# Kernel tuning notes

Hardware: AMD Instinct MI355X
Metric: run time of the kernel (lower is better)

## Reference

```python
import jax, jax.numpy as jnp
import numpy as np

NUM_NODES = 100000
NUM_EDGES = 50000
NUM_CONN = 800000
IN_DIM = 256
HIDDEN = 128
EDGE_ATTR_DIM = 17
LN_EPS = 1e-5


def setup_inputs() -> dict:
    key = jax.random.key(0)
    k1, k2, k3, kw1, kb1, kg, kbeta, kw2, kb2 = jax.random.split(key, 9)
    node_features = jax.random.normal(k1, (NUM_NODES, IN_DIM), dtype=jnp.float32)
    nodes = jax.random.randint(k2, (NUM_CONN,), 0, NUM_NODES, dtype=jnp.int64)
    edges = jax.random.randint(k3, (NUM_CONN,), 0, NUM_EDGES, dtype=jnp.int64)
    hyperedge_index = jnp.stack([nodes, edges], axis=0)
    # MLP params (Linear(in,hid) -> LayerNorm -> ReLU -> Dropout(eval:identity) -> Linear(hid,out))
    W1 = jax.random.normal(kw1, (IN_DIM, HIDDEN), dtype=jnp.float32) * (1.0 / np.sqrt(IN_DIM))
    b1 = jax.random.normal(kb1, (HIDDEN,), dtype=jnp.float32) * 0.01
    ln_g = jnp.ones((HIDDEN,), dtype=jnp.float32)
    ln_b = jnp.zeros((HIDDEN,), dtype=jnp.float32)
    W2 = jax.random.normal(kw2, (HIDDEN, EDGE_ATTR_DIM), dtype=jnp.float32) * (1.0 / np.sqrt(HIDDEN))
    b2 = jax.random.normal(kb2, (EDGE_ATTR_DIM,), dtype=jnp.float32) * 0.01
    return {"node_features": node_features, "hyperedge_index": hyperedge_index,
            "W1": W1, "b1": b1, "ln_g": ln_g, "ln_b": ln_b, "W2": W2, "b2": b2}


def reference(node_features, hyperedge_index, W1, b1, ln_g, ln_b, W2, b2):
    nodes = hyperedge_index[0]
    edges = hyperedge_index[1]
    # indices are in-range by construction (torch valid_mask is all-True here)
    gathered = node_features[nodes]                         # [num_conn, in_dim]
    summed = jax.ops.segment_sum(gathered, edges, num_segments=NUM_EDGES)
    counts = jax.ops.segment_sum(jnp.ones(edges.shape, node_features.dtype), edges,
                                 num_segments=NUM_EDGES)
    edge_features = summed / jnp.clip(counts, 1.0)[:, None]  # mean aggregation
    # decoder MLP (dropout inactive in eval)
    h = edge_features @ W1 + b1
    mu = jnp.mean(h, axis=-1, keepdims=True)
    var = jnp.mean(jnp.square(h - mu), axis=-1, keepdims=True)
    h = (h - mu) * jax.lax.rsqrt(var + LN_EPS) * ln_g + ln_b
    h = jax.nn.relu(h)
    return h @ W2 + b2                                      # [num_edges, edge_attr_dim]
```

## Files before the change

### kernel.cpp

```cpp
#include <hip/hip_runtime.h>
#include <hip/hip_bf16.h>
#include <stdint.h>

#define NUM_NODES 100000
#define NUM_EDGES 50000
#define NUM_CONN  800000
#define IN_DIM    256
#define HIDDEN    128
#define EDGE_DIM  17
#define PAD       64
#define CSTRIDE   16

typedef __bf16 bf16x8 __attribute__((ext_vector_type(8)));
typedef float  f32x4  __attribute__((ext_vector_type(4)));


__global__ void prep_kernel(const float* __restrict__ W1, const float* __restrict__ W2,
                            __bf16* __restrict__ w1f, __bf16* __restrict__ w2f,
                            int* __restrict__ counts2) {
    int i = blockIdx.x * 256 + threadIdx.x;
    if (i < NUM_EDGES) {
        int4 z = {0, 0, 0, 0};
        int4* c4 = (int4*)(counts2 + (size_t)i * CSTRIDE);
        c4[0] = z; c4[1] = z; c4[2] = z; c4[3] = z;
    }
    if (i < 4096) {
        int lane = i & 63, t = (i >> 6) & 7, kc2 = i >> 9;
        int m = lane & 15, q = lane >> 4;
        int n = t * 16 + m;
        int kbase = kc2 * 32 + q * 8;
        __bf16* dst = w1f + (size_t)i * 8;
        #pragma unroll
        for (int ki = 0; ki < 8; ++ki)
            dst[ki] = (__bf16)W1[(size_t)(kbase + ki) * HIDDEN + n];
    } else if (i < 4608) {
        int f = i - 4096;
        int lane = f & 63, t = (f >> 6) & 1, ks = f >> 7;
        int m = lane & 15, q = lane >> 4;
        int n = t * 16 + m;
        int kbase = ks * 32 + q * 8;
        __bf16* dst = w2f + (size_t)f * 8;
        #pragma unroll
        for (int ki = 0; ki < 8; ++ki)
            dst[ki] = (n < EDGE_DIM) ? (__bf16)W2[(size_t)(kbase + ki) * EDGE_DIM + n]
                                     : (__bf16)0.0f;
    }
}

#define FRONT_BLOCKS 2346
__global__ __launch_bounds__(256, 4) void front_kernel(const int* __restrict__ idx,
        int stride, int* __restrict__ counts2, int* __restrict__ slots,
        const float* __restrict__ nf, const __bf16* __restrict__ w1f,
        __bf16* __restrict__ pbf) {
    __shared__ __align__(16) __bf16 lds_w[16384];
    const int nb = blockIdx.x / 3, r3 = blockIdx.x % 3;
    if (r3 == 1) {
        long c0 = ((long)nb * 256 + threadIdx.x) * 4;
        if (c0 < NUM_CONN) {
            int nd[4], ed[4];
            if (stride == 2) {
                #pragma unroll
                for (int k = 0; k < 2; ++k) {
                    int4 vn = ((const int4*)idx)[c0 / 2 + k];
                    int4 ve = ((const int4*)(idx + 2 * NUM_CONN))[c0 / 2 + k];
                    nd[2 * k] = vn.x; nd[2 * k + 1] = vn.z;
                    ed[2 * k] = ve.x; ed[2 * k + 1] = ve.z;
                }
            } else {
                #pragma unroll
                for (int k = 0; k < 4; ++k) {
                    nd[k] = idx[c0 + k];
                    ed[k] = idx[NUM_CONN + c0 + k];
                }
            }
            int pos[4];
            #pragma unroll
            for (int k = 0; k < 4; ++k)
                pos[k] = atomicAdd(&counts2[(size_t)ed[k] * CSTRIDE], 1);
            #pragma unroll
            for (int k = 0; k < 4; ++k)
                if (pos[k] < PAD) slots[(size_t)ed[k] * PAD + pos[k]] = nd[k];
        }
        return;
    }
    const int p = 2 * nb + (r3 == 2 ? 1 : 0);
    const int wave = threadIdx.x >> 6;
    const int lane = threadIdx.x & 63;
    const int m = lane & 15, q = lane >> 4;
    int row = p * 64 + wave * 16 + m;
    if (row >= NUM_NODES) row = NUM_NODES - 1;
    const float* ap = nf + (size_t)row * IN_DIM + q * 8;

    const uint4* src = (const uint4*)w1f;
    uint4* dst = (uint4*)lds_w;

    bf16x8 afr[8];
    {
        float4 a4[8];
        #pragma unroll
        for (int kc2 = 0; kc2 < 4; ++kc2) {
            a4[2 * kc2]     = *(const float4*)(ap + kc2 * 32);
            a4[2 * kc2 + 1] = *(const float4*)(ap + kc2 * 32 + 4);
        }
        #pragma unroll
        for (int i = threadIdx.x; i < 2048; i += 256) {
            int kc2 = i >> 8, tt = (i >> 6) & 3, l = i & 63;
            dst[i] = src[(kc2 * 8 + tt) * 64 + l];
        }
        #pragma unroll
        for (int kc2 = 0; kc2 < 4; ++kc2) {
            float4 f0 = a4[2 * kc2], f1 = a4[2 * kc2 + 1];
            afr[kc2][0] = (__bf16)f0.x; afr[kc2][1] = (__bf16)f0.y;
            afr[kc2][2] = (__bf16)f0.z; afr[kc2][3] = (__bf16)f0.w;
            afr[kc2][4] = (__bf16)f1.x; afr[kc2][5] = (__bf16)f1.y;
            afr[kc2][6] = (__bf16)f1.z; afr[kc2][7] = (__bf16)f1.w;
        }
        #pragma unroll
        for (int kc2 = 4; kc2 < 8; ++kc2) {
            a4[2 * (kc2 - 4)]     = *(const float4*)(ap + kc2 * 32);
            a4[2 * (kc2 - 4) + 1] = *(const float4*)(ap + kc2 * 32 + 4);
        }
        #pragma unroll
        for (int kc2 = 4; kc2 < 8; ++kc2) {
            float4 f0 = a4[2 * (kc2 - 4)], f1 = a4[2 * (kc2 - 4) + 1];
            afr[kc2][0] = (__bf16)f0.x; afr[kc2][1] = (__bf16)f0.y;
            afr[kc2][2] = (__bf16)f0.z; afr[kc2][3] = (__bf16)f0.w;
            afr[kc2][4] = (__bf16)f1.x; afr[kc2][5] = (__bf16)f1.y;
            afr[kc2][6] = (__bf16)f1.z; afr[kc2][7] = (__bf16)f1.w;
        }
    }
    __syncthreads();

    const bf16x8* frag = (const bf16x8*)lds_w;
    #pragma unroll
    for (int ph = 0; ph < 2; ++ph) {
        f32x4 acc[4];
        #pragma unroll
        for (int tt = 0; tt < 4; ++tt) acc[tt] = (f32x4){0.f, 0.f, 0.f, 0.f};
        #pragma unroll
        for (int kc2 = 0; kc2 < 8; ++kc2) {
            #pragma unroll
            for (int tt = 0; tt < 4; ++tt)
                acc[tt] = __builtin_amdgcn_mfma_f32_16x16x32_bf16(
                    afr[kc2], frag[(kc2 * 4 + tt) * 64 + lane], acc[tt], 0, 0, 0);
        }
        int ob = p * 64 + wave * 16 + q * 4;
        #pragma unroll
        for (int tt = 0; tt < 4; ++tt) {
            int col = (ph * 4 + tt) * 16 + m;
            #pragma unroll
            for (int r = 0; r < 4; ++r) {
                int orow = ob + r;
                if (orow < NUM_NODES)
                    pbf[(size_t)orow * HIDDEN + col] = (__bf16)acc[tt][r];
            }
        }
        if (ph == 0) {
            __syncthreads();
            #pragma unroll
            for (int i = threadIdx.x; i < 2048; i += 256) {
                int kc2 = i >> 8, tt = (i >> 6) & 3, l = i & 63;
                dst[i] = src[(kc2 * 8 + 4 + tt) * 64 + l];
            }
            __syncthreads();
        }
    }
}

__global__ __launch_bounds__(256) void edge_kernel(const uint4* __restrict__ p4,
        const int* __restrict__ counts2, const int* __restrict__ slots,
        const float* __restrict__ b1, const float* __restrict__ ln_g,
        const float* __restrict__ ln_b, const __bf16* __restrict__ w2f,
        const float* __restrict__ b2, float* __restrict__ out) {
    __shared__ __align__(16) uint4 lds_r[256];
    const int wave = threadIdx.x >> 6;
    const int lane = threadIdx.x & 63;
    const int g = lane & 15, ge = lane >> 4;
    const int el = wave * 4 + ge;
    const int e = blockIdx.x * 16 + el;

    const int c = counts2[(size_t)e * CSTRIDE];
    const int cc = c < PAD ? c : PAD;
    const float inv = 1.0f / (float)(c > 0 ? c : 1);

    float acc[8];
    #pragma unroll
    for (int d = 0; d < 8; ++d) acc[d] = 0.f;

    for (int c0 = 0; c0 < cc; c0 += 16) {
        int slv = slots[(size_t)e * PAD + c0 + g];
        int lim = cc - c0; if (lim > 16) lim = 16;
        if (lim == 16) {
            #pragma unroll
            for (int k0 = 0; k0 < 16; k0 += 4) {
                uint4 u[4];
                #pragma unroll
                for (int k = 0; k < 4; ++k) {
                    int nd = __shfl(slv, ge * 16 + k0 + k, 64);
                    u[k] = p4[(size_t)nd * 16 + g];
                }
                #pragma unroll
                for (int k = 0; k < 4; ++k) {
                    acc[0] += __uint_as_float(u[k].x << 16);
                    acc[1] += __uint_as_float(u[k].x & 0xffff0000u);
                    acc[2] += __uint_as_float(u[k].y << 16);
                    acc[3] += __uint_as_float(u[k].y & 0xffff0000u);
                    acc[4] += __uint_as_float(u[k].z << 16);
                    acc[5] += __uint_as_float(u[k].z & 0xffff0000u);
                    acc[6] += __uint_as_float(u[k].w << 16);
                    acc[7] += __uint_as_float(u[k].w & 0xffff0000u);
                }
            }
        } else {
            for (int k0 = 0; k0 < lim; k0 += 4) {
                uint4 u[4];
                unsigned okm[4];
                #pragma unroll
                for (int k = 0; k < 4; ++k) {
                    int nd = __shfl(slv, ge * 16 + k0 + k, 64);
                    nd = ((unsigned)nd < NUM_NODES) ? nd : 0;
                    u[k] = p4[(size_t)nd * 16 + g];
                    okm[k] = (k0 + k < lim) ? 0xffffffffu : 0u;
                }
                #pragma unroll
                for (int k = 0; k < 4; ++k) {
                    uint4 v = u[k];
                    v.x &= okm[k]; v.y &= okm[k]; v.z &= okm[k]; v.w &= okm[k];
                    acc[0] += __uint_as_float(v.x << 16);
                    acc[1] += __uint_as_float(v.x & 0xffff0000u);
                    acc[2] += __uint_as_float(v.y << 16);
                    acc[3] += __uint_as_float(v.y & 0xffff0000u);
                    acc[4] += __uint_as_float(v.z << 16);
                    acc[5] += __uint_as_float(v.z & 0xffff0000u);
                    acc[6] += __uint_as_float(v.w << 16);
                    acc[7] += __uint_as_float(v.w & 0xffff0000u);
                }
            }
        }
    }

    float4 bA = ((const float4*)b1)[2 * g];
    float4 bB = ((const float4*)b1)[2 * g + 1];
    float h[8];
    h[0] = acc[0] * inv + bA.x; h[1] = acc[1] * inv + bA.y;
    h[2] = acc[2] * inv + bA.z; h[3] = acc[3] * inv + bA.w;
    h[4] = acc[4] * inv + bB.x; h[5] = acc[5] * inv + bB.y;
    h[6] = acc[6] * inv + bB.z; h[7] = acc[7] * inv + bB.w;

    float s = 0.f;
    #pragma unroll
    for (int d = 0; d < 8; ++d) s += h[d];
    #pragma unroll
    for (int off = 8; off > 0; off >>= 1) s += __shfl_xor(s, off, 64);
    float mu = s * (1.0f / 128.0f);

    float dv[8], vv = 0.f;
    #pragma unroll
    for (int d = 0; d < 8; ++d) { dv[d] = h[d] - mu; vv += dv[d] * dv[d]; }
    #pragma unroll
    for (int off = 8; off > 0; off >>= 1) vv += __shfl_xor(vv, off, 64);
    float rs = rsqrtf(vv * (1.0f / 128.0f) + 1e-5f);

    float4 gA = ((const float4*)ln_g)[2 * g];
    float4 gB = ((const float4*)ln_g)[2 * g + 1];
    float4 eA = ((const float4*)ln_b)[2 * g];
    float4 eB = ((const float4*)ln_b)[2 * g + 1];
    float gg[8] = {gA.x, gA.y, gA.z, gA.w, gB.x, gB.y, gB.z, gB.w};
    float ee[8] = {eA.x, eA.y, eA.z, eA.w, eB.x, eB.y, eB.z, eB.w};
    union { __bf16 b[8]; uint4 u; } pk;
    #pragma unroll
    for (int d = 0; d < 8; ++d) {
        float r = dv[d] * rs * gg[d] + ee[d];
        pk.b[d] = (__bf16)(r > 0.f ? r : 0.f);
    }
    lds_r[el * 16 + g] = pk.u;
    __syncthreads();

    if (wave == 0) {
        const int m = lane & 15, q = lane >> 4;
        const __bf16* lr = (const __bf16*)lds_r;
        const bf16x8* fw = (const bf16x8*)w2f;
        f32x4 a0 = (f32x4){0.f, 0.f, 0.f, 0.f};
        f32x4 a1 = (f32x4){0.f, 0.f, 0.f, 0.f};
        #pragma unroll
        for (int ks = 0; ks < 4; ++ks) {
            bf16x8 a = *(const bf16x8*)(lr + m * 128 + ks * 32 + q * 8);
            a0 = __builtin_amdgcn_mfma_f32_16x16x32_bf16(a, fw[(ks * 2 + 0) * 64 + lane], a0, 0, 0, 0);
            a1 = __builtin_amdgcn_mfma_f32_16x16x32_bf16(a, fw[(ks * 2 + 1) * 64 + lane], a1, 0, 0, 0);
        }
        int rowb = blockIdx.x * 16 + q * 4;
        float bm = b2[m];
        float b16 = b2[16];
        #pragma unroll
        for (int r = 0; r < 4; ++r) {
            out[(size_t)(rowb + r) * EDGE_DIM + m] = a0[r] + bm;
            if (m == 0) out[(size_t)(rowb + r) * EDGE_DIM + 16] = a1[r] + b16;
        }
    }
}

extern "C" void kernel_launch(void* const* d_in, const int* in_sizes, int n_in,
                              void* d_out, int out_size, void* d_ws, size_t ws_size,
                              hipStream_t stream) {
    const float* nf  = (const float*)d_in[0];
    const int*   idx = (const int*)d_in[1];
    const float* W1  = (const float*)d_in[2];
    const float* b1  = (const float*)d_in[3];
    const float* g   = (const float*)d_in[4];
    const float* be  = (const float*)d_in[5];
    const float* W2  = (const float*)d_in[6];
    const float* b2  = (const float*)d_in[7];
    float* out = (float*)d_out;

    char* ws = (char*)d_ws;
    __bf16* P       = (__bf16*)ws;
    int*    counts2 = (int*)(ws + 25600000);
    int*    slots   = (int*)(ws + 28800000);
    __bf16* W1F     = (__bf16*)(ws + 41600000);
    __bf16* W2F     = (__bf16*)(ws + 41665536);

    int stride = (in_sizes[1] == 2 * NUM_CONN) ? 1 : 2;

    prep_kernel<<<196, 256, 0, stream>>>(W1, W2, W1F, W2F, counts2);
    front_kernel<<<FRONT_BLOCKS, 256, 0, stream>>>(idx, stride, counts2, slots, nf, W1F, P);
    edge_kernel<<<NUM_EDGES / 16, 256, 0, stream>>>((const uint4*)P, counts2, slots,
                                                    b1, g, be, W2F, b2, out);
}
```

Measured before the change: 234.3 us.

## Read W1 fragments from global and stage output tile in LDS for coalesced stores

The front GEMM no longer copies W1 fragments into LDS in two phases with barriers. Each wave now reads its B fragments directly from global memory, which is small and likely cache-resident. The LDS is reused to hold the 64x128 bf16 output tile with a padded stride. Threads then write whole rows with 16-byte vector stores instead of scattered 2-byte stores, cutting the store transaction count and removing two barriers. The cost is more global/L2 traffic for the weights on every block.

```diff
diff --git a/kernel.cpp b/kernel.cpp
--- a/kernel.cpp
+++ b/kernel.cpp
@@ -48,11 +48,12 @@
 }
 
 #define FRONT_BLOCKS 2346
+#define LDS_STRIDE 136
 __global__ __launch_bounds__(256, 4) void front_kernel(const int* __restrict__ idx,
         int stride, int* __restrict__ counts2, int* __restrict__ slots,
         const float* __restrict__ nf, const __bf16* __restrict__ w1f,
         __bf16* __restrict__ pbf) {
-    __shared__ __align__(16) __bf16 lds_w[16384];
+    __shared__ __align__(16) __bf16 lds_p[64 * LDS_STRIDE];
     const int nb = blockIdx.x / 3, r3 = blockIdx.x % 3;
     if (r3 == 1) {
         long c0 = ((long)nb * 256 + threadIdx.x) * 4;
@@ -91,9 +92,6 @@
     if (row >= NUM_NODES) row = NUM_NODES - 1;
     const float* ap = nf + (size_t)row * IN_DIM + q * 8;
 
-    const uint4* src = (const uint4*)w1f;
-    uint4* dst = (uint4*)lds_w;
-
     bf16x8 afr[8];
     {
         float4 a4[8];
@@ -101,11 +99,6 @@
         for (int kc2 = 0; kc2 < 4; ++kc2) {
             a4[2 * kc2]     = *(const float4*)(ap + kc2 * 32);
             a4[2 * kc2 + 1] = *(const float4*)(ap + kc2 * 32 + 4);
-        }
-        #pragma unroll
-        for (int i = threadIdx.x; i < 2048; i += 256) {
-            int kc2 = i >> 8, tt = (i >> 6) & 3, l = i & 63;
-            dst[i] = src[(kc2 * 8 + tt) * 64 + l];
         }
         #pragma unroll
         for (int kc2 = 0; kc2 < 4; ++kc2) {
@@ -129,9 +122,8 @@
             afr[kc2][6] = (__bf16)f1.z; afr[kc2][7] = (__bf16)f1.w;
         }
     }
-    __syncthreads();
-
-    const bf16x8* frag = (const bf16x8*)lds_w;
+
+    const bf16x8* __restrict__ frag = (const bf16x8*)w1f;
     #pragma unroll
     for (int ph = 0; ph < 2; ++ph) {
         f32x4 acc[4];
@@ -142,27 +134,29 @@
             #pragma unroll
             for (int tt = 0; tt < 4; ++tt)
                 acc[tt] = __builtin_amdgcn_mfma_f32_16x16x32_bf16(
-                    afr[kc2], frag[(kc2 * 4 + tt) * 64 + lane], acc[tt], 0, 0, 0);
-        }
-        int ob = p * 64 + wave * 16 + q * 4;
+                    afr[kc2], frag[(kc2 * 8 + ph * 4 + tt) * 64 + lane], acc[tt], 0, 0, 0);
+        }
         #pragma unroll
         for (int tt = 0; tt < 4; ++tt) {
             int col = (ph * 4 + tt) * 16 + m;
-            #pragma unroll
-            for (int r = 0; r < 4; ++r) {
-                int orow = ob + r;
-                if (orow < NUM_NODES)
-                    pbf[(size_t)orow * HIDDEN + col] = (__bf16)acc[tt][r];
+            int rl = wave * 16 + q * 4;
+            #pragma unroll
+            for (int r = 0; r < 4; ++r)
+                lds_p[(rl + r) * LDS_STRIDE + col] = (__bf16)acc[tt][r];
+        }
+    }
+    __syncthreads();
+    {
+        const int j = threadIdx.x;
+        const int rl = j >> 2;
+        const int grow = p * 64 + rl;
+        if (grow < NUM_NODES) {
+            #pragma unroll
+            for (int it = 0; it < 4; ++it) {
+                int c = (j & 3) + 4 * it;
+                uint4 v = *(const uint4*)(lds_p + rl * LDS_STRIDE + c * 8);
+                *(uint4*)(pbf + (size_t)grow * HIDDEN + c * 8) = v;
             }
-        }
-        if (ph == 0) {
-            __syncthreads();
-            #pragma unroll
-            for (int i = threadIdx.x; i < 2048; i += 256) {
-                int kc2 = i >> 8, tt = (i >> 6) & 3, l = i & 63;
-                dst[i] = src[(kc2 * 8 + 4 + tt) * 64 + l];
-            }
-            __syncthreads();
         }
     }
 }
```

After: 250.8 us. 1.07x slower.

## Make front GEMM blocks loop over eight row tiles per W1 half with prefetch

Applied to the files above, without the earlier changes.

Front-kernel GEMM blocks change from one 64-row tile covering both W1 halves to eight 64-row tiles for a single 64-column half of W1. That half is staged into LDS once per block, and the next tile's node features are prefetched during the MFMA work. Scatter blocks now handle 8 connections per thread using vectorized index loads, and the grid shrinks with fewer waves per SIMD allowed. The trade-off is that each node-feature row is now read by two blocks, one per W1 half, which may double HBM traffic unless adjacent blocks share it through cache; an initial redundant feature load is also left in.

```diff
diff --git a/kernel.cpp b/kernel.cpp
--- a/kernel.cpp
+++ b/kernel.cpp
@@ -47,20 +47,19 @@
     }
 }
 
-#define FRONT_BLOCKS 2346
-__global__ __launch_bounds__(256, 4) void front_kernel(const int* __restrict__ idx,
+#define FRONT_BLOCKS 784
+__global__ __launch_bounds__(256, 2) void front_kernel(const int* __restrict__ idx,
         int stride, int* __restrict__ counts2, int* __restrict__ slots,
         const float* __restrict__ nf, const __bf16* __restrict__ w1f,
         __bf16* __restrict__ pbf) {
     __shared__ __align__(16) __bf16 lds_w[16384];
-    const int nb = blockIdx.x / 3, r3 = blockIdx.x % 3;
-    if (r3 == 1) {
-        long c0 = ((long)nb * 256 + threadIdx.x) * 4;
+    if (blockIdx.x & 1) {
+        long c0 = ((long)(blockIdx.x >> 1) * 256 + threadIdx.x) * 8;
         if (c0 < NUM_CONN) {
-            int nd[4], ed[4];
+            int nd[8], ed[8];
             if (stride == 2) {
                 #pragma unroll
-                for (int k = 0; k < 2; ++k) {
+                for (int k = 0; k < 4; ++k) {
                     int4 vn = ((const int4*)idx)[c0 / 2 + k];
                     int4 ve = ((const int4*)(idx + 2 * NUM_CONN))[c0 / 2 + k];
                     nd[2 * k] = vn.x; nd[2 * k + 1] = vn.z;
@@ -68,72 +67,97 @@
                 }
             } else {
                 #pragma unroll
-                for (int k = 0; k < 4; ++k) {
-                    nd[k] = idx[c0 + k];
-                    ed[k] = idx[NUM_CONN + c0 + k];
-                }
-            }
-            int pos[4];
-            #pragma unroll
-            for (int k = 0; k < 4; ++k)
+                for (int k = 0; k < 2; ++k) {
+                    int4 vn = ((const int4*)idx)[c0 / 4 + k];
+                    int4 ve = ((const int4*)(idx + NUM_CONN))[c0 / 4 + k];
+                    nd[4 * k] = vn.x; nd[4 * k + 1] = vn.y;
+                    nd[4 * k + 2] = vn.z; nd[4 * k + 3] = vn.w;
+                    ed[4 * k] = ve.x; ed[4 * k + 1] = ve.y;
+                    ed[4 * k + 2] = ve.z; ed[4 * k + 3] = ve.w;
+                }
+            }
+            int pos[8];
+            #pragma unroll
+            for (int k = 0; k < 8; ++k)
                 pos[k] = atomicAdd(&counts2[(size_t)ed[k] * CSTRIDE], 1);
             #pragma unroll
-            for (int k = 0; k < 4; ++k)
+            for (int k = 0; k < 8; ++k)
                 if (pos[k] < PAD) slots[(size_t)ed[k] * PAD + pos[k]] = nd[k];
         }
         return;
     }
-    const int p = 2 * nb + (r3 == 2 ? 1 : 0);
+    const int pid = blockIdx.x >> 1;
+    const int H = pid & 1;
+    const int rg = pid >> 1;
     const int wave = threadIdx.x >> 6;
     const int lane = threadIdx.x & 63;
     const int m = lane & 15, q = lane >> 4;
-    int row = p * 64 + wave * 16 + m;
-    if (row >= NUM_NODES) row = NUM_NODES - 1;
-    const float* ap = nf + (size_t)row * IN_DIM + q * 8;
-
-    const uint4* src = (const uint4*)w1f;
-    uint4* dst = (uint4*)lds_w;
-
-    bf16x8 afr[8];
+    const int row0 = rg * 512 + wave * 16 + m;
+
     {
-        float4 a4[8];
-        #pragma unroll
-        for (int kc2 = 0; kc2 < 4; ++kc2) {
-            a4[2 * kc2]     = *(const float4*)(ap + kc2 * 32);
-            a4[2 * kc2 + 1] = *(const float4*)(ap + kc2 * 32 + 4);
-        }
+        const uint4* src = (const uint4*)w1f;
+        uint4* dst = (uint4*)lds_w;
         #pragma unroll
         for (int i = threadIdx.x; i < 2048; i += 256) {
             int kc2 = i >> 8, tt = (i >> 6) & 3, l = i & 63;
-            dst[i] = src[(kc2 * 8 + tt) * 64 + l];
-        }
-        #pragma unroll
-        for (int kc2 = 0; kc2 < 4; ++kc2) {
-            float4 f0 = a4[2 * kc2], f1 = a4[2 * kc2 + 1];
-            afr[kc2][0] = (__bf16)f0.x; afr[kc2][1] = (__bf16)f0.y;
-            afr[kc2][2] = (__bf16)f0.z; afr[kc2][3] = (__bf16)f0.w;
-            afr[kc2][4] = (__bf16)f1.x; afr[kc2][5] = (__bf16)f1.y;
-            afr[kc2][6] = (__bf16)f1.z; afr[kc2][7] = (__bf16)f1.w;
-        }
-        #pragma unroll
-        for (int kc2 = 4; kc2 < 8; ++kc2) {
-            a4[2 * (kc2 - 4)]     = *(const float4*)(ap + kc2 * 32);
-            a4[2 * (kc2 - 4) + 1] = *(const float4*)(ap + kc2 * 32 + 4);
-        }
-        #pragma unroll
-        for (int kc2 = 4; kc2 < 8; ++kc2) {
-            float4 f0 = a4[2 * (kc2 - 4)], f1 = a4[2 * (kc2 - 4) + 1];
-            afr[kc2][0] = (__bf16)f0.x; afr[kc2][1] = (__bf16)f0.y;
-            afr[kc2][2] = (__bf16)f0.z; afr[kc2][3] = (__bf16)f0.w;
-            afr[kc2][4] = (__bf16)f1.x; afr[kc2][5] = (__bf16)f1.y;
-            afr[kc2][6] = (__bf16)f1.z; afr[kc2][7] = (__bf16)f1.w;
+            dst[i] = src[(kc2 * 8 + H * 4 + tt) * 64 + l];
+        }
+    }
+    float4 a4[8];
+    {
+        int r = row0;
+        if (r >= NUM_NODES) r = NUM_NODES - 1;
+        const float* ap = nf + (size_t)r * IN_DIM + q * 8;
+        #pragma unroll
+        for (int kc2 = 0; kc2 < 8; ++kc2) {
+            a4[2 * (kc2 & 3)]     = *(const float4*)(ap + kc2 * 32);
+            a4[2 * (kc2 & 3) + 1] = *(const float4*)(ap + kc2 * 32 + 4);
+            if (kc2 == 3) {  }
         }
     }
     __syncthreads();
 
     const bf16x8* frag = (const bf16x8*)lds_w;
-    #pragma unroll
-    for (int ph = 0; ph < 2; ++ph) {
+
+    {
+        int r = row0;
+        if (r >= NUM_NODES) r = NUM_NODES - 1;
+        const float* ap = nf + (size_t)r * IN_DIM + q * 8;
+        #pragma unroll
+        for (int kc2 = 0; kc2 < 8; ++kc2) {
+            a4[kc2] = *(const float4*)(ap + kc2 * 32);
+        }
+    }
+
+    #pragma unroll 1
+    for (int t = 0; t < 8; ++t) {
+        bf16x8 afr[8];
+        {
+            int r = row0 + t * 64;
+            if (r >= NUM_NODES) r = NUM_NODES - 1;
+            const float* ap = nf + (size_t)r * IN_DIM + q * 8;
+            float4 b4[8];
+            #pragma unroll
+            for (int kc2 = 0; kc2 < 8; ++kc2)
+                b4[kc2] = *(const float4*)(ap + kc2 * 32 + 4);
+            #pragma unroll
+            for (int kc2 = 0; kc2 < 8; ++kc2) {
+                float4 f0 = a4[kc2], f1 = b4[kc2];
+                afr[kc2][0] = (__bf16)f0.x; afr[kc2][1] = (__bf16)f0.y;
+                afr[kc2][2] = (__bf16)f0.z; afr[kc2][3] = (__bf16)f0.w;
+                afr[kc2][4] = (__bf16)f1.x; afr[kc2][5] = (__bf16)f1.y;
+                afr[kc2][6] = (__bf16)f1.z; afr[kc2][7] = (__bf16)f1.w;
+            }
+        }
+        if (t < 7) {
+            int r = row0 + (t + 1) * 64;
+            if (r >= NUM_NODES) r = NUM_NODES - 1;
+            const float* ap = nf + (size_t)r * IN_DIM + q * 8;
+            #pragma unroll
+            for (int kc2 = 0; kc2 < 8; ++kc2)
+                a4[kc2] = *(const float4*)(ap + kc2 * 32);
+        }
+
         f32x4 acc[4];
         #pragma unroll
         for (int tt = 0; tt < 4; ++tt) acc[tt] = (f32x4){0.f, 0.f, 0.f, 0.f};
@@ -144,25 +168,17 @@
                 acc[tt] = __builtin_amdgcn_mfma_f32_16x16x32_bf16(
                     afr[kc2], frag[(kc2 * 4 + tt) * 64 + lane], acc[tt], 0, 0, 0);
         }
-        int ob = p * 64 + wave * 16 + q * 4;
+
+        const int ob = rg * 512 + t * 64 + wave * 16 + q * 4;
         #pragma unroll
         for (int tt = 0; tt < 4; ++tt) {
-            int col = (ph * 4 + tt) * 16 + m;
+            int col = H * 64 + tt * 16 + m;
             #pragma unroll
             for (int r = 0; r < 4; ++r) {
                 int orow = ob + r;
                 if (orow < NUM_NODES)
                     pbf[(size_t)orow * HIDDEN + col] = (__bf16)acc[tt][r];
             }
-        }
-        if (ph == 0) {
-            __syncthreads();
-            #pragma unroll
-            for (int i = threadIdx.x; i < 2048; i += 256) {
-                int kc2 = i >> 8, tt = (i >> 6) & 3, l = i & 63;
-                dst[i] = src[(kc2 * 8 + 4 + tt) * 64 + l];
-            }
-            __syncthreads();
         }
     }
 }
```

Result: slower. 281.6 us (+20.2%).

## Widen front kernel to 512 threads and load full W1 into LDS once

Applied to the files above, without the earlier changes.

The fused scatter/GEMM front kernel now uses 512-thread blocks. Each GEMM block handles 128 node rows and keeps the whole 64KB bf16 W1 fragment in LDS, so the two-phase reload and its extra barriers go away. Blocks alternate between scatter and GEMM roles, and scatter blocks process 2 connections per thread. Each thread holds 8 accumulator tiles at once, which raises register pressure, and the larger LDS footprint may cut occupancy.

```diff
diff --git a/kernel.cpp b/kernel.cpp
--- a/kernel.cpp
+++ b/kernel.cpp
@@ -47,47 +47,42 @@
     }
 }
 
-#define FRONT_BLOCKS 2346
-__global__ __launch_bounds__(256, 4) void front_kernel(const int* __restrict__ idx,
+#define FRONT_BLOCKS 1564
+__global__ __launch_bounds__(512, 4) void front_kernel(const int* __restrict__ idx,
         int stride, int* __restrict__ counts2, int* __restrict__ slots,
         const float* __restrict__ nf, const __bf16* __restrict__ w1f,
         __bf16* __restrict__ pbf) {
-    __shared__ __align__(16) __bf16 lds_w[16384];
-    const int nb = blockIdx.x / 3, r3 = blockIdx.x % 3;
-    if (r3 == 1) {
-        long c0 = ((long)nb * 256 + threadIdx.x) * 4;
+    __shared__ __align__(16) __bf16 lds_w[32768];
+    if (blockIdx.x & 1) {
+        long c0 = ((long)(blockIdx.x >> 1) * 512 + threadIdx.x) * 2;
         if (c0 < NUM_CONN) {
-            int nd[4], ed[4];
+            int nd[2], ed[2];
             if (stride == 2) {
-                #pragma unroll
-                for (int k = 0; k < 2; ++k) {
-                    int4 vn = ((const int4*)idx)[c0 / 2 + k];
-                    int4 ve = ((const int4*)(idx + 2 * NUM_CONN))[c0 / 2 + k];
-                    nd[2 * k] = vn.x; nd[2 * k + 1] = vn.z;
-                    ed[2 * k] = ve.x; ed[2 * k + 1] = ve.z;
-                }
+                int4 vn = ((const int4*)idx)[c0 / 2];
+                int4 ve = ((const int4*)(idx + 2 * NUM_CONN))[c0 / 2];
+                nd[0] = vn.x; nd[1] = vn.z;
+                ed[0] = ve.x; ed[1] = ve.z;
             } else {
-                #pragma unroll
-                for (int k = 0; k < 4; ++k) {
-                    nd[k] = idx[c0 + k];
-                    ed[k] = idx[NUM_CONN + c0 + k];
-                }
+                int2 vn = ((const int2*)idx)[c0 / 2];
+                int2 ve = ((const int2*)(idx + NUM_CONN))[c0 / 2];
+                nd[0] = vn.x; nd[1] = vn.y;
+                ed[0] = ve.x; ed[1] = ve.y;
             }
-            int pos[4];
+            int pos[2];
             #pragma unroll
-            for (int k = 0; k < 4; ++k)
+            for (int k = 0; k < 2; ++k)
                 pos[k] = atomicAdd(&counts2[(size_t)ed[k] * CSTRIDE], 1);
             #pragma unroll
-            for (int k = 0; k < 4; ++k)
+            for (int k = 0; k < 2; ++k)
                 if (pos[k] < PAD) slots[(size_t)ed[k] * PAD + pos[k]] = nd[k];
         }
         return;
     }
-    const int p = 2 * nb + (r3 == 2 ? 1 : 0);
+    const int pid = blockIdx.x >> 1;
     const int wave = threadIdx.x >> 6;
     const int lane = threadIdx.x & 63;
     const int m = lane & 15, q = lane >> 4;
-    int row = p * 64 + wave * 16 + m;
+    int row = pid * 128 + wave * 16 + m;
     if (row >= NUM_NODES) row = NUM_NODES - 1;
     const float* ap = nf + (size_t)row * IN_DIM + q * 8;
 
@@ -103,10 +98,8 @@
             a4[2 * kc2 + 1] = *(const float4*)(ap + kc2 * 32 + 4);
         }
         #pragma unroll
-        for (int i = threadIdx.x; i < 2048; i += 256) {
-            int kc2 = i >> 8, tt = (i >> 6) & 3, l = i & 63;
-            dst[i] = src[(kc2 * 8 + tt) * 64 + l];
-        }
+        for (int i = threadIdx.x; i < 4096; i += 512)
+            dst[i] = src[i];
         #pragma unroll
         for (int kc2 = 0; kc2 < 4; ++kc2) {
             float4 f0 = a4[2 * kc2], f1 = a4[2 * kc2 + 1];
@@ -132,37 +125,25 @@
     __syncthreads();
 
     const bf16x8* frag = (const bf16x8*)lds_w;
-    #pragma unroll
-    for (int ph = 0; ph < 2; ++ph) {
-        f32x4 acc[4];
-        #pragma unroll
-        for (int tt = 0; tt < 4; ++tt) acc[tt] = (f32x4){0.f, 0.f, 0.f, 0.f};
-        #pragma unroll
-        for (int kc2 = 0; kc2 < 8; ++kc2) {
-            #pragma unroll
-            for (int tt = 0; tt < 4; ++tt)
-                acc[tt] = __builtin_amdgcn_mfma_f32_16x16x32_bf16(
-                    afr[kc2], frag[(kc2 * 4 + tt) * 64 + lane], acc[tt], 0, 0, 0);
-        }
-        int ob = p * 64 + wave * 16 + q * 4;
-        #pragma unroll
-        for (int tt = 0; tt < 4; ++tt) {
-            int col = (ph * 4 + tt) * 16 + m;
-            #pragma unroll
-            for (int r = 0; r < 4; ++r) {
-                int orow = ob + r;
-                if (orow < NUM_NODES)
-                    pbf[(size_t)orow * HIDDEN + col] = (__bf16)acc[tt][r];
-            }
-        }
-        if (ph == 0) {
-            __syncthreads();
-            #pragma unroll
-            for (int i = threadIdx.x; i < 2048; i += 256) {
-                int kc2 = i >> 8, tt = (i >> 6) & 3, l = i & 63;
-                dst[i] = src[(kc2 * 8 + 4 + tt) * 64 + l];
-            }
-            __syncthreads();
+    f32x4 acc[8];
+    #pragma unroll
+    for (int tt = 0; tt < 8; ++tt) acc[tt] = (f32x4){0.f, 0.f, 0.f, 0.f};
+    #pragma unroll
+    for (int kc2 = 0; kc2 < 8; ++kc2) {
+        #pragma unroll
+        for (int tt = 0; tt < 8; ++tt)
+            acc[tt] = __builtin_amdgcn_mfma_f32_16x16x32_bf16(
+                afr[kc2], frag[(kc2 * 8 + tt) * 64 + lane], acc[tt], 0, 0, 0);
+    }
+    const int ob = pid * 128 + wave * 16 + q * 4;
+    #pragma unroll
+    for (int tt = 0; tt < 8; ++tt) {
+        int col = tt * 16 + m;
+        #pragma unroll
+        for (int r = 0; r < 4; ++r) {
+            int orow = ob + r;
+            if (orow < NUM_NODES)
+                pbf[(size_t)orow * HIDDEN + col] = (__bf16)acc[tt][r];
         }
     }
 }
@@ -322,7 +303,7 @@
     int stride = (in_sizes[1] == 2 * NUM_CONN) ? 1 : 2;
 
     prep_kernel<<<196, 256, 0, stream>>>(W1, W2, W1F, W2F, counts2);
-    front_kernel<<<FRONT_BLOCKS, 256, 0, stream>>>(idx, stride, counts2, slots, nf, W1F, P);
+    front_kernel<<<FRONT_BLOCKS, 512, 0, stream>>>(idx, stride, counts2, slots, nf, W1F, P);
     edge_kernel<<<NUM_EDGES / 16, 256, 0, stream>>>((const uint4*)P, counts2, slots,
                                                     b1, g, be, W2F, b2, out);
 }
```

Measured after the change: 237.6 us. About the same (+1.4%).
